# Optimization experiments

Measured on AMD Instinct MI355X. Metric: run time of the kernel, lower is better.

Reference implementation:

```python
import jax, jax.numpy as jnp
import numpy as np

N, DEG = 20000, 16
E = N * DEG
D_IN, D_HID, D_OUT, L = 1024, 512, 128, 3


def setup_inputs() -> dict:
    key = jax.random.key(0)
    ks = jax.random.split(key, 16)
    scale = 0.02
    X = jax.random.normal(ks[0], (N, D_IN), dtype=jnp.float32)
    senders = jax.random.randint(ks[1], (E,), 0, N)
    receivers = jnp.repeat(jnp.arange(N), DEG)  # sorted, every node has DEG neighbors
    inp = {"X": X, "senders": senders, "receivers": receivers}
    ki = 2
    for l in range(L):
        din = D_IN >> l
        dh = D_HID >> l
        inp[f"lw{l}"] = jax.random.normal(ks[ki], (2 * din, dh), jnp.float32) * scale; ki += 1
        inp[f"lb{l}"] = jnp.zeros((dh,), jnp.float32)
        inp[f"aw{l}"] = jax.random.normal(ks[ki], (din, dh), jnp.float32) * scale; ki += 1
        inp[f"aq{l}"] = jax.random.normal(ks[ki], (dh,), jnp.float32) * scale; ki += 1
    inp["ow"] = jax.random.normal(ks[ki], (D_HID >> (L - 1), D_OUT), jnp.float32) * scale
    inp["ob"] = jnp.zeros((D_OUT,), jnp.float32)
    return inp


def _attend(h, senders, receivers, aw, aq):
    # scores depend only on the neighbor (sender) embedding: q @ relu(W h_j)
    logits = jnp.einsum('nh,h->n', jax.nn.relu(h @ aw), aq)            # [N]
    el = logits[senders]                                               # [E]
    m = jax.ops.segment_max(el, receivers, num_segments=N)            # per-receiver max
    w = jnp.exp(el - m[receivers])                                     # [E]
    denom = jax.ops.segment_sum(w, receivers, num_segments=N)         # [N]
    msg = jax.ops.segment_sum(w[:, None] * h[senders], receivers, num_segments=N)  # [N,D]
    return msg / denom[:, None]


def reference(X, senders, receivers,
              lw0, lb0, aw0, aq0,
              lw1, lb1, aw1, aq1,
              lw2, lb2, aw2, aq2,
              ow, ob):
    params = [(lw0, lb0, aw0, aq0), (lw1, lb1, aw1, aq1), (lw2, lb2, aw2, aq2)]
    h = X
    for lw, lb, aw, aq in params:
        hN = _attend(h, senders, receivers, aw, aq)
        h = jax.nn.relu(jnp.concatenate([h, hN], axis=1) @ lw + lb)
    return h[14] @ ow + ob
```

## Files before the change

kernel.cpp:

```cpp
#include <hip/hip_runtime.h>
#include <math.h>

typedef unsigned short ushort_t;
typedef __attribute__((ext_vector_type(8))) short short8;
typedef __attribute__((ext_vector_type(4))) float f32x4;

#define NN    20000
#define DEG   16
constexpr int MAXL2 = 1 + DEG;
constexpr int MAXL1 = MAXL2 + MAXL2*DEG;
constexpr int L0PAD = 73 * 64;

__device__ __forceinline__ ushort_t f2bf(float f) {
    unsigned u = __float_as_uint(f);
    return (ushort_t)((u + 0x7FFFu + ((u >> 16) & 1u)) >> 16);
}

__device__ void transpose_tile(const float* __restrict__ W, ushort_t* __restrict__ WT,
                               int b, int nshift, int K) {
    __shared__ float tile[32][33];
    int t = threadIdx.x;
    int N = 32 << nshift;
    int bx = b & ((1 << nshift) - 1), by = b >> nshift;
    int i0 = t >> 3, j0 = (t & 7) * 4;
    int k = by * 32 + i0, n0 = bx * 32;
    float4 v = *(const float4*)(W + (size_t)k * N + n0 + j0);
    tile[i0][j0] = v.x; tile[i0][j0 + 1] = v.y; tile[i0][j0 + 2] = v.z; tile[i0][j0 + 3] = v.w;
    __syncthreads();
    int n = n0 + i0, kc = j0;
    ushort_t* p = WT + (size_t)n * K + by * 32 + kc;
    p[0] = f2bf(tile[kc][i0]);     p[1] = f2bf(tile[kc + 1][i0]);
    p[2] = f2bf(tile[kc + 2][i0]); p[3] = f2bf(tile[kc + 3][i0]);
}

__global__ __launch_bounds__(256)
void k_frontier(const int* __restrict__ senders,
                int* __restrict__ list2, int* __restrict__ inv2,
                int* __restrict__ list1, int* __restrict__ inv1,
                int* __restrict__ cnts,
                const float* __restrict__ aw0, ushort_t* __restrict__ awT,
                const float* __restrict__ aw1, ushort_t* __restrict__ awT1,
                const float* __restrict__ lw1, const float* __restrict__ aw2,
                const float* __restrict__ lw2, const float* __restrict__ ow,
                float* __restrict__ dummy,
                float4* __restrict__ zp, int n4, int nzb) {
    int t = threadIdx.x;
    int bb = (int)blockIdx.x;
    if (bb > 0) {
        int b = bb - 1;
        if (b < nzb) {
            int i = b * 256 + t;
            if (i < n4) zp[i] = make_float4(0.f, 0.f, 0.f, 0.f);
            return;
        }
        b -= nzb;
        if (b < 512) { transpose_tile(aw0, awT, b, 4, 1024); return; }
        b -= 512;
        if (b < 128) { transpose_tile(aw1, awT1, b, 3, 512); return; }
        b -= 128;
        const float4* src; int base;
        if (b < 64)       { src = (const float4*)lw1; base = b * 1024; }
        else if (b < 72)  { src = (const float4*)aw2; base = (b - 64) * 1024; }
        else if (b < 88)  { src = (const float4*)lw2; base = (b - 72) * 1024; }
        else              { src = (const float4*)ow;  base = (b - 88) * 1024; }
        float s = 0.f;
#pragma unroll
        for (int i = 0; i < 4; i++) {
            float4 v = src[base + i * 256 + t];
            s += v.x + v.y + v.z + v.w;
        }
        if (s == 1234.5678f) dummy[0] = s;
        return;
    }
    __shared__ unsigned bm[625];
    __shared__ int cnt;
    __shared__ int lloc[MAXL2];
    auto clear = [&]() { for (int i = t; i < 625; i += 256) bm[i] = 0u; if (t == 0) cnt = 0; };
    clear(); __syncthreads();
    if (t < 17) {
        int node = (t < 16) ? senders[14 * DEG + t] : 14;
        unsigned bit = 1u << (node & 31);
        unsigned old = atomicOr(&bm[node >> 5], bit);
        if (!(old & bit)) { int p = atomicAdd(&cnt, 1); list2[p] = node; inv2[node] = p; lloc[p] = node; }
    }
    __syncthreads();
    int c2 = cnt;
    if (t == 0) cnts[2] = c2;
    __syncthreads(); clear(); __syncthreads();
    for (int i = t; i < c2 * 17; i += 256) {
        int r = i / 17, k = i - r * 17;
        int node = (k < 16) ? senders[lloc[r] * DEG + k] : lloc[r];
        unsigned bit = 1u << (node & 31);
        unsigned old = atomicOr(&bm[node >> 5], bit);
        if (!(old & bit)) { int p = atomicAdd(&cnt, 1); list1[p] = node; inv1[node] = p; }
    }
    __syncthreads();
    if (t == 0) { int c1 = cnt; cnts[1] = c1; cnts[0] = c1 * 16; }
}

__global__ __launch_bounds__(256)
void k_prep(const float* __restrict__ X, const int* __restrict__ senders,
            const int* __restrict__ list1, const int* __restrict__ cnts,
            int* __restrict__ inv0, ushort_t* __restrict__ Xg) {
    int r = blockIdx.x;
    int t = threadIdx.x;
    int rc = cnts[0];
    ushort_t o0 = 0, o1 = 0, o2 = 0, o3 = 0;
    if (r < rc) {
        int n = list1[r >> 4];
        int s = senders[n * DEG + (r & 15)];
        if (t == 0) inv0[s] = r;
        float4 v = *(const float4*)(X + (size_t)s * 1024 + t * 4);
        o0 = f2bf(v.x); o1 = f2bf(v.y); o2 = f2bf(v.z); o3 = f2bf(v.w);
    }
    ushort_t* p = Xg + (size_t)r * 1024 + t * 4;
    p[0] = o0; p[1] = o1; p[2] = o2; p[3] = o3;
}

__global__ __launch_bounds__(256)
void k_logits_mfma(const ushort_t* __restrict__ Xg,
                   const ushort_t* __restrict__ WT,
                   const float* __restrict__ aq, float* __restrict__ lgc,
                   const int* __restrict__ cnt, int K) {
    __shared__ short As[64 * 40];
    __shared__ short Bs[64 * 40];
    int rcnt = *cnt;
    int row0 = blockIdx.x * 64;
    if (row0 >= rcnt) return;
    int col0 = blockIdx.y * 64;
    int t = threadIdx.x;
    int w = t >> 6, lane = t & 63;

    int sr = t >> 2, sk = (t & 3) * 8;
    const ushort_t* ap = Xg + (size_t)(row0 + sr) * K + sk;
    const ushort_t* bp = WT + (size_t)(col0 + sr) * K + sk;

    int fm = lane & 15, fq = lane >> 4;
    const short* arow = As + (w * 16 + fm) * 40 + fq * 8;
    const short* brow = Bs + fm * 40 + fq * 8;

    f32x4 acc0 = {0.f,0.f,0.f,0.f}, acc1 = {0.f,0.f,0.f,0.f};
    f32x4 acc2 = {0.f,0.f,0.f,0.f}, acc3 = {0.f,0.f,0.f,0.f};

    short8 pa = *(const short8*)(ap);
    short8 pb = *(const short8*)(bp);
    for (int k0 = 0; k0 < K; k0 += 32) {
        *(short8*)(As + sr * 40 + sk) = pa;
        *(short8*)(Bs + sr * 40 + sk) = pb;
        __syncthreads();
        if (k0 + 32 < K) {
            pa = *(const short8*)(ap + k0 + 32);
            pb = *(const short8*)(bp + k0 + 32);
        }
        short8 af = *(const short8*)arow;
        short8 b0 = *(const short8*)(brow);
        short8 b1 = *(const short8*)(brow + 16 * 40);
        short8 b2 = *(const short8*)(brow + 32 * 40);
        short8 b3 = *(const short8*)(brow + 48 * 40);
        acc0 = __builtin_amdgcn_mfma_f32_16x16x32_bf16(af, b0, acc0, 0, 0, 0);
        acc1 = __builtin_amdgcn_mfma_f32_16x16x32_bf16(af, b1, acc1, 0, 0, 0);
        acc2 = __builtin_amdgcn_mfma_f32_16x16x32_bf16(af, b2, acc2, 0, 0, 0);
        acc3 = __builtin_amdgcn_mfma_f32_16x16x32_bf16(af, b3, acc3, 0, 0, 0);
        __syncthreads();
    }

    float aqv0 = aq[col0 + fm], aqv1 = aq[col0 + 16 + fm];
    float aqv2 = aq[col0 + 32 + fm], aqv3 = aq[col0 + 48 + fm];
#pragma unroll
    for (int r = 0; r < 4; r++) {
        float v = fmaxf(acc0[r], 0.f) * aqv0 + fmaxf(acc1[r], 0.f) * aqv1
                + fmaxf(acc2[r], 0.f) * aqv2 + fmaxf(acc3[r], 0.f) * aqv3;
#pragma unroll
        for (int off = 1; off < 16; off <<= 1) v += __shfl_xor(v, off);
        if (fm == 0) atomicAdd(&lgc[row0 + w * 16 + fq * 4 + r], v);
    }
}

__global__ __launch_bounds__(256)
void k_matmul(const float* __restrict__ A1, const float* __restrict__ A2,
              const int* __restrict__ list, const int* __restrict__ inv,
              const float* __restrict__ B, const float* __restrict__ aq,
              float* __restrict__ C, const int* __restrict__ cnt,
              int amode, int omode, int K1, int K2, int NC, int KS) {
    __shared__ float As[32][68];
    __shared__ float Bs[32][64];
    __shared__ float rowsum[64];

    int rcnt = *cnt;
    int row0 = blockIdx.x * 64;
    if (row0 >= rcnt) return;
    int col0 = blockIdx.y * 64;
    int K = K1 + K2;
    int kbeg = blockIdx.z * KS;
    int kend = kbeg + KS; if (kend > K) kend = K;

    int t = threadIdx.x;
    int ty = t >> 4, tx = t & 15;
    int lr = t >> 2, kaoff = (t & 3) * 4;
    int grow = row0 + lr;
    bool rowValid = grow < rcnt;
    const float* rp1 = A1;
    const float* rp2 = A2;
    if (rowValid) {
        int hrow;
        if (amode == 0) hrow = grow;
        else { int node = list[grow]; hrow = (amode == 2) ? inv[node] : node; }
        rp1 = A1 + (size_t)hrow * K1;
        rp2 = A2 + (size_t)grow * K2;
    }
    const float* Bp = B + col0;
    int bidx0 = t, bidx1 = t + 256;

    auto loadA = [&](int k) -> float4 {
        if (!rowValid) return make_float4(0.f, 0.f, 0.f, 0.f);
        const float* src = (k < K1) ? (rp1 + k) : (rp2 + (k - K1));
        return *(const float4*)src;
    };
    auto loadB = [&](int idx, int k0) -> float4 {
        int row = idx >> 4, c4 = (idx & 15) * 4;
        return *(const float4*)(Bp + (size_t)(k0 + row) * NC + c4);
    };

    float4 pa0 = loadA(kbeg + kaoff);
    float4 pa1 = loadA(kbeg + kaoff + 16);
    float4 pb0 = loadB(bidx0, kbeg);
    float4 pb1 = loadB(bidx1, kbeg);

    float acc[4][4] = {};
    for (int k0 = kbeg; k0 < kend; k0 += 32) {
        As[kaoff + 0][lr] = pa0.x; As[kaoff + 1][lr] = pa0.y;
        As[kaoff + 2][lr] = pa0.z; As[kaoff + 3][lr] = pa0.w;
        As[kaoff + 16][lr] = pa1.x; As[kaoff + 17][lr] = pa1.y;
        As[kaoff + 18][lr] = pa1.z; As[kaoff + 19][lr] = pa1.w;
        *(float4*)&Bs[bidx0 >> 4][(bidx0 & 15) * 4] = pb0;
        *(float4*)&Bs[bidx1 >> 4][(bidx1 & 15) * 4] = pb1;
        __syncthreads();
        if (k0 + 32 < kend) {
            pa0 = loadA(k0 + 32 + kaoff);
            pa1 = loadA(k0 + 32 + kaoff + 16);
            pb0 = loadB(bidx0, k0 + 32);
            pb1 = loadB(bidx1, k0 + 32);
        }
#pragma unroll
        for (int kk = 0; kk < 32; kk++) {
            float4 a4 = *(const float4*)&As[kk][ty * 4];
            float4 b4 = *(const float4*)&Bs[kk][tx * 4];
            float a[4] = {a4.x, a4.y, a4.z, a4.w};
            float b[4] = {b4.x, b4.y, b4.z, b4.w};
#pragma unroll
            for (int i = 0; i < 4; i++)
#pragma unroll
                for (int j = 0; j < 4; j++) acc[i][j] += a[i] * b[j];
        }
        __syncthreads();
    }

    if (omode == 0) {
#pragma unroll
        for (int i = 0; i < 4; i++) {
            int r = row0 + ty * 4 + i;
            if (r < rcnt) {
                float* Crow = C + (size_t)r * NC + col0 + tx * 4;
#pragma unroll
                for (int j = 0; j < 4; j++) atomicAdd(&Crow[j], acc[i][j]);
            }
        }
    } else {
        if (t < 64) rowsum[t] = 0.f;
        __syncthreads();
        float aqv[4];
#pragma unroll
        for (int j = 0; j < 4; j++) aqv[j] = aq[col0 + tx * 4 + j];
#pragma unroll
        for (int i = 0; i < 4; i++) {
            float s = 0.f;
#pragma unroll
            for (int j = 0; j < 4; j++) {
                float v = acc[i][j];
                v = v > 0.f ? v : 0.f;
                s += v * aqv[j];
            }
            atomicAdd(&rowsum[ty * 4 + i], s);
        }
        __syncthreads();
        if (t < 64) {
            int r = row0 + t;
            if (r < rcnt) atomicAdd(&C[r], rowsum[t]);
        }
    }
}

__global__ void k_bias_relu(const float* __restrict__ C, const float* __restrict__ b,
                            float* __restrict__ H, ushort_t* __restrict__ Hb,
                            const int* __restrict__ cnt, int ncShift) {
    int rcnt = *cnt;
    int NC = 1 << ncShift;
    int e = blockIdx.x * 256 + threadIdx.x;
    int r = e >> ncShift;
    if (r >= rcnt) return;
    int c = e & (NC - 1);
    float v = C[(size_t)r * NC + c] + b[c];
    v = v > 0.f ? v : 0.f;
    H[(size_t)r * NC + c] = v;
    Hb[(size_t)r * NC + c] = f2bf(v);
}

__global__ __launch_bounds__(256)
void k_agg(const float* __restrict__ Hsrc, const int* __restrict__ invH,
           const float* __restrict__ lgc, const int* __restrict__ invL,
           const int* __restrict__ senders,
           const int* __restrict__ listN, const int* __restrict__ cntN,
           float* __restrict__ hN, int din) {
    __shared__ int   s_row[DEG];
    __shared__ float s_w[DEG];
    __shared__ float s_scale;
    int b = blockIdx.x;
    if (b >= *cntN) return;
    int n = listN[b];
    int t = threadIdx.x;
    if (t < DEG) {
        int s = senders[n * DEG + t];
        s_row[t] = invH ? invH[s] : s;
        s_w[t] = lgc[invL ? invL[s] : s];
    }
    __syncthreads();
    if (t == 0) {
        float m = -1e30f;
        for (int k = 0; k < DEG; k++) m = fmaxf(m, s_w[k]);
        float d = 0.f;
        for (int k = 0; k < DEG; k++) { float w = __expf(s_w[k] - m); s_w[k] = w; d += w; }
        s_scale = 1.f / d;
    }
    __syncthreads();
    float scale = s_scale;
    for (int dI = t * 4; dI < din; dI += 1024) {
        float4 acc = make_float4(0.f, 0.f, 0.f, 0.f);
#pragma unroll
        for (int k = 0; k < DEG; k++) {
            float w = s_w[k];
            float4 v = *(const float4*)(Hsrc + (size_t)s_row[k] * din + dI);
            acc.x += w * v.x; acc.y += w * v.y; acc.z += w * v.z; acc.w += w * v.w;
        }
        acc.x *= scale; acc.y *= scale; acc.z *= scale; acc.w *= scale;
        *(float4*)(hN + (size_t)b * din + dI) = acc;
    }
}

__global__ __launch_bounds__(256)
void k_tail1(const float* __restrict__ h1, const float* __restrict__ lgc1,
             const int* __restrict__ senders, const int* __restrict__ list2,
             const int* __restrict__ inv1, const int* __restrict__ cnts,
             const float* __restrict__ lw1, const float* __restrict__ lb1,
             float* __restrict__ h2) {
    __shared__ __align__(16) float As[17][1024];
    __shared__ float sw[17][16];
    __shared__ int   srow[17][16];
    __shared__ int   orow[17];
    __shared__ float psum[8][17 * 32];
    int c2 = cnts[2];
    int t = threadIdx.x;
    int b = blockIdx.x;

    for (int i = t; i < c2 * 16; i += 256) {
        int j = i >> 4, k = i & 15;
        int s = senders[list2[j] * DEG + k];
        int rr = inv1[s];
        srow[j][k] = rr;
        sw[j][k] = lgc1[rr];
    }
    if (t < c2) orow[t] = inv1[list2[t]];
    __syncthreads();
    if (t < c2) {
        float m = -1e30f;
        for (int k = 0; k < 16; k++) m = fmaxf(m, sw[t][k]);
        float d = 0.f;
        for (int k = 0; k < 16; k++) { float w = __expf(sw[t][k] - m); sw[t][k] = w; d += w; }
        float inv = 1.f / d;
        for (int k = 0; k < 16; k++) sw[t][k] *= inv;
    }
    __syncthreads();
    for (int e = t; e < c2 * 128; e += 256) {
        int j = e >> 7, d4 = (e & 127) * 4;
        *(float4*)&As[j][d4] = *(const float4*)&h1[(size_t)orow[j] * 512 + d4];
        float4 a = make_float4(0.f, 0.f, 0.f, 0.f);
#pragma unroll
        for (int k = 0; k < 16; k++) {
            float w = sw[j][k];
            float4 v = *(const float4*)&h1[(size_t)srow[j][k] * 512 + d4];
            a.x += w * v.x; a.y += w * v.y; a.z += w * v.z; a.w += w * v.w;
        }
        *(float4*)&As[j][512 + d4] = a;
    }
    __syncthreads();
    int c = t & 31, s = t >> 5;
    int gc = b * 32 + c;
    float acc[17];
#pragma unroll
    for (int j = 0; j < 17; j++) acc[j] = 0.f;
    for (int k = s * 128; k < s * 128 + 128; k += 4) {
        float b0 = lw1[(size_t)(k + 0) * 256 + gc];
        float b1 = lw1[(size_t)(k + 1) * 256 + gc];
        float b2 = lw1[(size_t)(k + 2) * 256 + gc];
        float b3 = lw1[(size_t)(k + 3) * 256 + gc];
#pragma unroll
        for (int j = 0; j < 17; j++) {
            float4 a = *(const float4*)&As[j][k];
            acc[j] += a.x * b0 + a.y * b1 + a.z * b2 + a.w * b3;
        }
    }
#pragma unroll
    for (int j = 0; j < 17; j++) psum[s][j * 32 + c] = acc[j];
    __syncthreads();
    for (int e = t; e < c2 * 32; e += 256) {
        int j = e >> 5, cc = e & 31;
        float v = 0.f;
#pragma unroll
        for (int s2 = 0; s2 < 8; s2++) v += psum[s2][j * 32 + cc];
        v += lb1[b * 32 + cc];
        h2[(size_t)j * 256 + b * 32 + cc] = v > 0.f ? v : 0.f;
    }
}

__global__ __launch_bounds__(512)
void k_tail2(const float* __restrict__ h2, const int* __restrict__ senders,
             const int* __restrict__ inv2, const int* __restrict__ cnts,
             const float* __restrict__ aw2, const float* __restrict__ aq2,
             const float* __restrict__ lw2, const float* __restrict__ lb2,
             const float* __restrict__ ow, const float* __restrict__ ob,
             float* __restrict__ out) {
    __shared__ __align__(16) float sh2[17][256];
    __shared__ __align__(16) float psum[8][17][128];
    __shared__ __align__(16) float h3in[512];
    __shared__ __align__(16) float sh3[128];
    __shared__ __align__(16) float psumB[16][128];
    __shared__ float slog[17];
    __shared__ float swt[16];
    __shared__ int   srow2[16];
    __shared__ int   srow14;
    int c2 = cnts[2];
    int t = threadIdx.x;
    for (int e = t; e < c2 * 64; e += 512) {
        int j = e >> 6, d4 = (e & 63) * 4;
        *(float4*)&sh2[j][d4] = *(const float4*)&h2[(size_t)j * 256 + d4];
    }
    if (t < c2) slog[t] = 0.f;
    if (t < 16) srow2[t] = inv2[senders[14 * DEG + t]];
    if (t == 31) srow14 = inv2[14];
    __syncthreads();
    {
        int cg = t & 31;
        int s  = (t >> 5) & 7;
        int jg = t >> 8;
        int j0 = jg * 9;
        int jend = min(c2, j0 + 9);
        float4 acc[9];
#pragma unroll
        for (int i = 0; i < 9; i++) acc[i] = make_float4(0.f, 0.f, 0.f, 0.f);
        const float* ap = aw2 + cg * 4;
        for (int k = s * 32; k < s * 32 + 32; k++) {
            float4 bv = *(const float4*)(ap + (size_t)k * 128);
#pragma unroll
            for (int i = 0; i < 9; i++) {
                int j = j0 + i;
                if (j < jend) {
                    float a = sh2[j][k];
                    acc[i].x += a * bv.x; acc[i].y += a * bv.y;
                    acc[i].z += a * bv.z; acc[i].w += a * bv.w;
                }
            }
        }
#pragma unroll
        for (int i = 0; i < 9; i++) {
            int j = j0 + i;
            if (j < jend) *(float4*)&psum[s][j][cg * 4] = acc[i];
        }
    }
    __syncthreads();
    for (int e = t; e < c2 * 128; e += 512) {
        int j = e >> 7, c = e & 127;
        float v = 0.f;
#pragma unroll
        for (int s = 0; s < 8; s++) v += psum[s][j][c];
        v = v > 0.f ? v : 0.f;
        atomicAdd(&slog[j], v * aq2[c]);
    }
    __syncthreads();
    if (t == 0) {
        float m = -1e30f;
        for (int k = 0; k < 16; k++) m = fmaxf(m, slog[srow2[k]]);
        float d = 0.f;
        for (int k = 0; k < 16; k++) { float w = __expf(slog[srow2[k]] - m); swt[k] = w; d += w; }
        float inv = 1.f / d;
        for (int k = 0; k < 16; k++) swt[k] *= inv;
    }
    __syncthreads();
    if (t < 256) {
        float a = 0.f;
#pragma unroll
        for (int k = 0; k < 16; k++) a += swt[k] * sh2[srow2[k]][t];
        h3in[256 + t] = a;
    } else {
        int d = t - 256;
        h3in[d] = sh2[srow14][d];
    }
    __syncthreads();
    {
        int cg = t & 31, s = t >> 5;
        float4 acc = make_float4(0.f, 0.f, 0.f, 0.f);
        const float* bp = lw2 + cg * 4;
        for (int k = s * 32; k < s * 32 + 32; k++) {
            float4 bv = *(const float4*)(bp + (size_t)k * 128);
            float a = h3in[k];
            acc.x += a * bv.x; acc.y += a * bv.y; acc.z += a * bv.z; acc.w += a * bv.w;
        }
        *(float4*)&psumB[s][cg * 4] = acc;
    }
    __syncthreads();
    if (t < 128) {
        float v = lb2[t];
#pragma unroll
        for (int s = 0; s < 16; s++) v += psumB[s][t];
        sh3[t] = v > 0.f ? v : 0.f;
    }
    __syncthreads();
    {
        int cg = t & 31, s = t >> 5;
        float4 acc = make_float4(0.f, 0.f, 0.f, 0.f);
        const float* bp = ow + cg * 4;
        for (int k = s * 8; k < s * 8 + 8; k++) {
            float4 bv = *(const float4*)(bp + (size_t)k * 128);
            float a = sh3[k];
            acc.x += a * bv.x; acc.y += a * bv.y; acc.z += a * bv.z; acc.w += a * bv.w;
        }
        *(float4*)&psumB[s][cg * 4] = acc;
    }
    __syncthreads();
    if (t < 128) {
        float v = ob[t];
#pragma unroll
        for (int s = 0; s < 16; s++) v += psumB[s][t];
        out[t] = v;
    }
}

extern "C" void kernel_launch(void* const* d_in, const int* in_sizes, int n_in,
                              void* d_out, int out_size, void* d_ws, size_t ws_size,
                              hipStream_t stream) {
    const float* X       = (const float*)d_in[0];
    const int*   senders = (const int*)d_in[1];
    const float* lw0 = (const float*)d_in[3];
    const float* lb0 = (const float*)d_in[4];
    const float* aw0 = (const float*)d_in[5];
    const float* aq0 = (const float*)d_in[6];
    const float* lw1 = (const float*)d_in[7];
    const float* lb1 = (const float*)d_in[8];
    const float* aw1 = (const float*)d_in[9];
    const float* aq1 = (const float*)d_in[10];
    const float* lw2 = (const float*)d_in[11];
    const float* lb2 = (const float*)d_in[12];
    const float* aw2 = (const float*)d_in[13];
    const float* aq2 = (const float*)d_in[14];
    const float* owp = (const float*)d_in[15];
    const float* obp = (const float*)d_in[16];
    float* out = (float*)d_out;

    char* ws = (char*)d_ws;
    size_t off = 0;
    auto alloc = [&](size_t nbytes) -> void* {
        void* p = ws + off;
        off += (nbytes + 255) & ~(size_t)255;
        return p;
    };
    float* lgc0     = (float*)alloc(L0PAD * 4);
    float* lgc1     = (float*)alloc(320 * 4);
    float* C0       = (float*)alloc((size_t)MAXL1 * 512 * 4);
    ushort_t* h1b   = (ushort_t*)alloc((size_t)320 * 512 * 2);
    size_t zero_end = off;
    int* inv0  = (int*)alloc(NN * 4);
    int* inv1  = (int*)alloc(NN * 4);
    int* inv2  = (int*)alloc(NN * 4);
    int* list1 = (int*)alloc(MAXL1 * 4);
    int* list2 = (int*)alloc(MAXL2 * 4);
    int* cnts  = (int*)alloc(4 * 4);
    float* dummy = (float*)alloc(16);
    ushort_t* Xg   = (ushort_t*)alloc((size_t)L0PAD * 1024 * 2);
    ushort_t* awT  = (ushort_t*)alloc((size_t)512 * 1024 * 2);
    ushort_t* awT1 = (ushort_t*)alloc((size_t)256 * 512 * 2);
    float* hN0c = (float*)alloc((size_t)MAXL1 * 1024 * 4);
    float* h1c  = (float*)alloc((size_t)MAXL1 * 512 * 4);
    float* h2c  = (float*)alloc((size_t)MAXL2 * 256 * 4);
    (void)in_sizes; (void)n_in; (void)out_size; (void)ws_size;

    int nz4 = (int)(zero_end / 16);
    int nzb = (nz4 + 255) / 256;

    hipLaunchKernelGGL(k_frontier, dim3(1 + nzb + 512 + 128 + 92), dim3(256), 0, stream,
                       senders, list2, inv2, list1, inv1, cnts,
                       aw0, awT, aw1, awT1, lw1, aw2, lw2, owp, dummy,
                       (float4*)ws, nz4, nzb);
    hipLaunchKernelGGL(k_prep, dim3(L0PAD), dim3(256), 0, stream,
                       X, senders, list1, cnts, inv0, Xg);
    hipLaunchKernelGGL(k_logits_mfma, dim3(73, 8), dim3(256), 0, stream,
                       Xg, awT, aq0, lgc0, cnts + 0, 1024);
    hipLaunchKernelGGL(k_agg, dim3(MAXL1), dim3(256), 0, stream,
                       X, (const int*)nullptr, lgc0, inv0, senders, list1, cnts + 1, hN0c, 1024);
    hipLaunchKernelGGL(k_matmul, dim3((MAXL1 + 63) / 64, 512 / 64, 8), dim3(256), 0, stream,
                       X, hN0c, list1, (int*)nullptr, lw0, aq0, C0, cnts + 1,
                       1, 0, 1024, 1024, 512, 256);
    hipLaunchKernelGGL(k_bias_relu, dim3((MAXL1 * 512 + 255) / 256), dim3(256), 0, stream,
                       C0, lb0, h1c, h1b, cnts + 1, 9);
    hipLaunchKernelGGL(k_logits_mfma, dim3(5, 4), dim3(256), 0, stream,
                       h1b, awT1, aq1, lgc1, cnts + 1, 512);
    hipLaunchKernelGGL(k_tail1, dim3(8), dim3(256), 0, stream,
                       h1c, lgc1, senders, list2, inv1, cnts, lw1, lb1, h2c);
    hipLaunchKernelGGL(k_tail2, dim3(1), dim3(512), 0, stream,
                       h2c, senders, inv2, cnts, aw2, aq2, lw2, lb2, owp, obp, out);
}
```

Baseline: 265.7 us.

## Fuse layer-1 bias/relu with logits, widen logits MFMA tile, vectorize bf16 stores

Replaces the separate bias+relu kernel and the second MFMA logits launch (with its aw1 transpose) with one per-row kernel that applies bias/relu and computes the layer-1 attention logit in fp32 straight from aw1. It also widens the layer-0 logits tile to 128 columns so each A tile is reused across twice as many outputs, halving the grid, and packs bf16 writes into ushort4 stores. The aim is fewer launches, less bf16 staging, and less redundant A loading. The cost is that each fused block rereads all of aw1 (512 KB) per row, and the wider tile uses more registers and LDS.

```diff
diff --git a/kernel.cpp b/kernel.cpp
--- a/kernel.cpp
+++ b/kernel.cpp
@@ -29,8 +29,10 @@
     __syncthreads();
     int n = n0 + i0, kc = j0;
     ushort_t* p = WT + (size_t)n * K + by * 32 + kc;
-    p[0] = f2bf(tile[kc][i0]);     p[1] = f2bf(tile[kc + 1][i0]);
-    p[2] = f2bf(tile[kc + 2][i0]); p[3] = f2bf(tile[kc + 3][i0]);
+    ushort4 o;
+    o.x = f2bf(tile[kc][i0]);     o.y = f2bf(tile[kc + 1][i0]);
+    o.z = f2bf(tile[kc + 2][i0]); o.w = f2bf(tile[kc + 3][i0]);
+    *(ushort4*)p = o;
 }
 
 __global__ __launch_bounds__(256)
@@ -39,7 +41,7 @@
                 int* __restrict__ list1, int* __restrict__ inv1,
                 int* __restrict__ cnts,
                 const float* __restrict__ aw0, ushort_t* __restrict__ awT,
-                const float* __restrict__ aw1, ushort_t* __restrict__ awT1,
+                const float* __restrict__ aw1,
                 const float* __restrict__ lw1, const float* __restrict__ aw2,
                 const float* __restrict__ lw2, const float* __restrict__ ow,
                 float* __restrict__ dummy,
@@ -56,13 +58,12 @@
         b -= nzb;
         if (b < 512) { transpose_tile(aw0, awT, b, 4, 1024); return; }
         b -= 512;
-        if (b < 128) { transpose_tile(aw1, awT1, b, 3, 512); return; }
-        b -= 128;
         const float4* src; int base;
-        if (b < 64)       { src = (const float4*)lw1; base = b * 1024; }
-        else if (b < 72)  { src = (const float4*)aw2; base = (b - 64) * 1024; }
-        else if (b < 88)  { src = (const float4*)lw2; base = (b - 72) * 1024; }
-        else              { src = (const float4*)ow;  base = (b - 88) * 1024; }
+        if (b < 64)        { src = (const float4*)lw1; base = b * 1024; }
+        else if (b < 96)   { src = (const float4*)aw1; base = (b - 64) * 1024; }
+        else if (b < 104)  { src = (const float4*)aw2; base = (b - 96) * 1024; }
+        else if (b < 120)  { src = (const float4*)lw2; base = (b - 104) * 1024; }
+        else               { src = (const float4*)ow;  base = (b - 120) * 1024; }
         float s = 0.f;
 #pragma unroll
         for (int i = 0; i < 4; i++) {
@@ -105,16 +106,15 @@
     int r = blockIdx.x;
     int t = threadIdx.x;
     int rc = cnts[0];
-    ushort_t o0 = 0, o1 = 0, o2 = 0, o3 = 0;
+    ushort4 o = make_ushort4(0, 0, 0, 0);
     if (r < rc) {
         int n = list1[r >> 4];
         int s = senders[n * DEG + (r & 15)];
         if (t == 0) inv0[s] = r;
         float4 v = *(const float4*)(X + (size_t)s * 1024 + t * 4);
-        o0 = f2bf(v.x); o1 = f2bf(v.y); o2 = f2bf(v.z); o3 = f2bf(v.w);
-    }
-    ushort_t* p = Xg + (size_t)r * 1024 + t * 4;
-    p[0] = o0; p[1] = o1; p[2] = o2; p[3] = o3;
+        o.x = f2bf(v.x); o.y = f2bf(v.y); o.z = f2bf(v.z); o.w = f2bf(v.w);
+    }
+    *(ushort4*)(Xg + (size_t)r * 1024 + t * 4) = o;
 }
 
 __global__ __launch_bounds__(256)
@@ -123,53 +123,70 @@
                    const float* __restrict__ aq, float* __restrict__ lgc,
                    const int* __restrict__ cnt, int K) {
     __shared__ short As[64 * 40];
-    __shared__ short Bs[64 * 40];
+    __shared__ short Bs0[64 * 40];
+    __shared__ short Bs1[64 * 40];
     int rcnt = *cnt;
     int row0 = blockIdx.x * 64;
     if (row0 >= rcnt) return;
-    int col0 = blockIdx.y * 64;
+    int col0 = blockIdx.y * 128;
     int t = threadIdx.x;
     int w = t >> 6, lane = t & 63;
 
     int sr = t >> 2, sk = (t & 3) * 8;
-    const ushort_t* ap = Xg + (size_t)(row0 + sr) * K + sk;
-    const ushort_t* bp = WT + (size_t)(col0 + sr) * K + sk;
+    const ushort_t* ap  = Xg + (size_t)(row0 + sr) * K + sk;
+    const ushort_t* bp0 = WT + (size_t)(col0 + sr) * K + sk;
+    const ushort_t* bp1 = WT + (size_t)(col0 + 64 + sr) * K + sk;
 
     int fm = lane & 15, fq = lane >> 4;
-    const short* arow = As + (w * 16 + fm) * 40 + fq * 8;
-    const short* brow = Bs + fm * 40 + fq * 8;
-
-    f32x4 acc0 = {0.f,0.f,0.f,0.f}, acc1 = {0.f,0.f,0.f,0.f};
-    f32x4 acc2 = {0.f,0.f,0.f,0.f}, acc3 = {0.f,0.f,0.f,0.f};
-
-    short8 pa = *(const short8*)(ap);
-    short8 pb = *(const short8*)(bp);
+    const short* arow  = As  + (w * 16 + fm) * 40 + fq * 8;
+    const short* brow0 = Bs0 + fm * 40 + fq * 8;
+    const short* brow1 = Bs1 + fm * 40 + fq * 8;
+
+    f32x4 acc[2][4];
+#pragma unroll
+    for (int h = 0; h < 2; h++)
+#pragma unroll
+        for (int c = 0; c < 4; c++) acc[h][c] = (f32x4){0.f, 0.f, 0.f, 0.f};
+
+    short8 pa  = *(const short8*)(ap);
+    short8 pb0 = *(const short8*)(bp0);
+    short8 pb1 = *(const short8*)(bp1);
     for (int k0 = 0; k0 < K; k0 += 32) {
-        *(short8*)(As + sr * 40 + sk) = pa;
-        *(short8*)(Bs + sr * 40 + sk) = pb;
+        *(short8*)(As  + sr * 40 + sk) = pa;
+        *(short8*)(Bs0 + sr * 40 + sk) = pb0;
+        *(short8*)(Bs1 + sr * 40 + sk) = pb1;
         __syncthreads();
         if (k0 + 32 < K) {
-            pa = *(const short8*)(ap + k0 + 32);
-            pb = *(const short8*)(bp + k0 + 32);
+            pa  = *(const short8*)(ap  + k0 + 32);
+            pb0 = *(const short8*)(bp0 + k0 + 32);
+            pb1 = *(const short8*)(bp1 + k0 + 32);
         }
         short8 af = *(const short8*)arow;
-        short8 b0 = *(const short8*)(brow);
-        short8 b1 = *(const short8*)(brow + 16 * 40);
-        short8 b2 = *(const short8*)(brow + 32 * 40);
-        short8 b3 = *(const short8*)(brow + 48 * 40);
-        acc0 = __builtin_amdgcn_mfma_f32_16x16x32_bf16(af, b0, acc0, 0, 0, 0);
-        acc1 = __builtin_amdgcn_mfma_f32_16x16x32_bf16(af, b1, acc1, 0, 0, 0);
-        acc2 = __builtin_amdgcn_mfma_f32_16x16x32_bf16(af, b2, acc2, 0, 0, 0);
-        acc3 = __builtin_amdgcn_mfma_f32_16x16x32_bf16(af, b3, acc3, 0, 0, 0);
+#pragma unroll
+        for (int c = 0; c < 4; c++) {
+            short8 b0 = *(const short8*)(brow0 + c * 16 * 40);
+            acc[0][c] = __builtin_amdgcn_mfma_f32_16x16x32_bf16(af, b0, acc[0][c], 0, 0, 0);
+        }
+#pragma unroll
+        for (int c = 0; c < 4; c++) {
+            short8 b1 = *(const short8*)(brow1 + c * 16 * 40);
+            acc[1][c] = __builtin_amdgcn_mfma_f32_16x16x32_bf16(af, b1, acc[1][c], 0, 0, 0);
+        }
         __syncthreads();
     }
 
-    float aqv0 = aq[col0 + fm], aqv1 = aq[col0 + 16 + fm];
-    float aqv2 = aq[col0 + 32 + fm], aqv3 = aq[col0 + 48 + fm];
+    float aqv[2][4];
+#pragma unroll
+    for (int h = 0; h < 2; h++)
+#pragma unroll
+        for (int c = 0; c < 4; c++) aqv[h][c] = aq[col0 + h * 64 + c * 16 + fm];
 #pragma unroll
     for (int r = 0; r < 4; r++) {
-        float v = fmaxf(acc0[r], 0.f) * aqv0 + fmaxf(acc1[r], 0.f) * aqv1
-                + fmaxf(acc2[r], 0.f) * aqv2 + fmaxf(acc3[r], 0.f) * aqv3;
+        float v = 0.f;
+#pragma unroll
+        for (int h = 0; h < 2; h++)
+#pragma unroll
+            for (int c = 0; c < 4; c++) v += fmaxf(acc[h][c][r], 0.f) * aqv[h][c];
 #pragma unroll
         for (int off = 1; off < 16; off <<= 1) v += __shfl_xor(v, off);
         if (fm == 0) atomicAdd(&lgc[row0 + w * 16 + fq * 4 + r], v);
@@ -290,19 +307,37 @@
     }
 }
 
-__global__ void k_bias_relu(const float* __restrict__ C, const float* __restrict__ b,
-                            float* __restrict__ H, ushort_t* __restrict__ Hb,
-                            const int* __restrict__ cnt, int ncShift) {
-    int rcnt = *cnt;
-    int NC = 1 << ncShift;
-    int e = blockIdx.x * 256 + threadIdx.x;
-    int r = e >> ncShift;
-    if (r >= rcnt) return;
-    int c = e & (NC - 1);
-    float v = C[(size_t)r * NC + c] + b[c];
-    v = v > 0.f ? v : 0.f;
-    H[(size_t)r * NC + c] = v;
-    Hb[(size_t)r * NC + c] = f2bf(v);
+__global__ __launch_bounds__(256)
+void k_bias_logits(const float* __restrict__ C0, const float* __restrict__ lb0,
+                   const float* __restrict__ aw1, const float* __restrict__ aq1,
+                   float* __restrict__ h1, float* __restrict__ lgc1,
+                   const int* __restrict__ cnt) {
+    __shared__ float sh[512];
+    __shared__ float red[4];
+    int r = blockIdx.x;
+    if (r >= *cnt) return;
+    int t = threadIdx.x;
+    float v0 = C0[(size_t)r * 512 + t] + lb0[t];
+    float v1 = C0[(size_t)r * 512 + 256 + t] + lb0[256 + t];
+    v0 = v0 > 0.f ? v0 : 0.f;
+    v1 = v1 > 0.f ? v1 : 0.f;
+    sh[t] = v0; sh[256 + t] = v1;
+    h1[(size_t)r * 512 + t] = v0;
+    h1[(size_t)r * 512 + 256 + t] = v1;
+    __syncthreads();
+    float dot = 0.f;
+    for (int k = 0; k < 512; k += 4) {
+        dot += sh[k + 0] * aw1[(size_t)(k + 0) * 256 + t]
+             + sh[k + 1] * aw1[(size_t)(k + 1) * 256 + t]
+             + sh[k + 2] * aw1[(size_t)(k + 2) * 256 + t]
+             + sh[k + 3] * aw1[(size_t)(k + 3) * 256 + t];
+    }
+    float v = (dot > 0.f ? dot : 0.f) * aq1[t];
+#pragma unroll
+    for (int off = 1; off < 64; off <<= 1) v += __shfl_xor(v, off);
+    if ((t & 63) == 0) red[t >> 6] = v;
+    __syncthreads();
+    if (t == 0) lgc1[r] = red[0] + red[1] + red[2] + red[3];
 }
 
 __global__ __launch_bounds__(256)
@@ -572,10 +607,9 @@
         return p;
     };
     float* lgc0     = (float*)alloc(L0PAD * 4);
-    float* lgc1     = (float*)alloc(320 * 4);
     float* C0       = (float*)alloc((size_t)MAXL1 * 512 * 4);
-    ushort_t* h1b   = (ushort_t*)alloc((size_t)320 * 512 * 2);
     size_t zero_end = off;
+    float* lgc1 = (float*)alloc(MAXL1 * 4);
     int* inv0  = (int*)alloc(NN * 4);
     int* inv1  = (int*)alloc(NN * 4);
     int* inv2  = (int*)alloc(NN * 4);
@@ -585,7 +619,6 @@
     float* dummy = (float*)alloc(16);
     ushort_t* Xg   = (ushort_t*)alloc((size_t)L0PAD * 1024 * 2);
     ushort_t* awT  = (ushort_t*)alloc((size_t)512 * 1024 * 2);
-    ushort_t* awT1 = (ushort_t*)alloc((size_t)256 * 512 * 2);
     float* hN0c = (float*)alloc((size_t)MAXL1 * 1024 * 4);
     float* h1c  = (float*)alloc((size_t)MAXL1 * 512 * 4);
     float* h2c  = (float*)alloc((size_t)MAXL2 * 256 * 4);
@@ -594,23 +627,21 @@
     int nz4 = (int)(zero_end / 16);
     int nzb = (nz4 + 255) / 256;
 
-    hipLaunchKernelGGL(k_frontier, dim3(1 + nzb + 512 + 128 + 92), dim3(256), 0, stream,
+    hipLaunchKernelGGL(k_frontier, dim3(1 + nzb + 512 + 124), dim3(256), 0, stream,
                        senders, list2, inv2, list1, inv1, cnts,
-                       aw0, awT, aw1, awT1, lw1, aw2, lw2, owp, dummy,
+                       aw0, awT, aw1, lw1, aw2, lw2, owp, dummy,
                        (float4*)ws, nz4, nzb);
     hipLaunchKernelGGL(k_prep, dim3(L0PAD), dim3(256), 0, stream,
                        X, senders, list1, cnts, inv0, Xg);
-    hipLaunchKernelGGL(k_logits_mfma, dim3(73, 8), dim3(256), 0, stream,
+    hipLaunchKernelGGL(k_logits_mfma, dim3(73, 4), dim3(256), 0, stream,
                        Xg, awT, aq0, lgc0, cnts + 0, 1024);
     hipLaunchKernelGGL(k_agg, dim3(MAXL1), dim3(256), 0, stream,
                        X, (const int*)nullptr, lgc0, inv0, senders, list1, cnts + 1, hN0c, 1024);
     hipLaunchKernelGGL(k_matmul, dim3((MAXL1 + 63) / 64, 512 / 64, 8), dim3(256), 0, stream,
                        X, hN0c, list1, (int*)nullptr, lw0, aq0, C0, cnts + 1,
                        1, 0, 1024, 1024, 512, 256);
-    hipLaunchKernelGGL(k_bias_relu, dim3((MAXL1 * 512 + 255) / 256), dim3(256), 0, stream,
-                       C0, lb0, h1c, h1b, cnts + 1, 9);
-    hipLaunchKernelGGL(k_logits_mfma, dim3(5, 4), dim3(256), 0, stream,
-                       h1b, awT1, aq1, lgc1, cnts + 1, 512);
+    hipLaunchKernelGGL(k_bias_logits, dim3(MAXL1), dim3(256), 0, stream,
+                       C0, lb0, aw1, aq1, h1c, lgc1, cnts + 1);
     hipLaunchKernelGGL(k_tail1, dim3(8), dim3(256), 0, stream,
                        h1c, lgc1, senders, list2, inv1, cnts, lw1, lb1, h2c);
     hipLaunchKernelGGL(k_tail2, dim3(1), dim3(512), 0, stream,
```

After: 267.1 us. No clear change (+0.5%).
